# Kernel tuning notes

Hardware: AMD Instinct MI355X
Metric: run time of the kernel (lower is better)

Reference implementation:

```python
import jax, jax.numpy as jnp
import numpy as np

N_NODES = 100000
N_EDGES = 250000
EMB = 300
LAYERS = 5
BN_EPS = 1e-5


def setup_inputs() -> dict:
    key = jax.random.key(0)
    ks = jax.random.split(key, 16)
    inp = {
        "x": jax.random.randint(ks[0], (N_NODES, 2), 0, 3, dtype=jnp.int64) if jax.config.jax_enable_x64 else jax.random.randint(ks[0], (N_NODES, 2), 0, 3, dtype=jnp.int32),
        "edge_index": jax.random.randint(ks[1], (2, N_EDGES), 0, N_NODES, dtype=jnp.int32),
        "edge_attr": jax.random.randint(ks[2], (N_EDGES, 2), 0, 3, dtype=jnp.int32),
        "atom_emb1": jax.random.normal(ks[3], (120, EMB), jnp.float32) * 0.1,
        "atom_emb2": jax.random.normal(ks[4], (3, EMB), jnp.float32) * 0.1,
        "edge_emb1": jax.random.normal(ks[5], (LAYERS, 6, EMB), jnp.float32) * 0.1,
        "edge_emb2": jax.random.normal(ks[6], (LAYERS, 3, EMB), jnp.float32) * 0.1,
        "W1": jax.random.normal(ks[7], (LAYERS, EMB, 2 * EMB), jnp.float32) * (1.0 / np.sqrt(EMB)),
        "b1": jnp.zeros((LAYERS, 2 * EMB), jnp.float32),
        "W2": jax.random.normal(ks[8], (LAYERS, 2 * EMB, EMB), jnp.float32) * (1.0 / np.sqrt(2 * EMB)),
        "b2": jnp.zeros((LAYERS, EMB), jnp.float32),
        "gamma": jnp.ones((LAYERS, EMB), jnp.float32),
        "beta": jnp.zeros((LAYERS, EMB), jnp.float32),
    }
    return inp


def reference(x, edge_index, edge_attr, atom_emb1, atom_emb2, edge_emb1, edge_emb2,
              W1, b1, W2, b2, gamma, beta):
    N = x.shape[0]
    L = W1.shape[0]
    # AtomEncoder: sum of per-feature embeddings
    h = atom_emb1[x[:, 0]] + atom_emb2[x[:, 1]]  # [N, D]
    # add self loops (attr = (4, 0)); PyG: messages flow src=row0 -> dst=row1
    sl = jnp.arange(N, dtype=edge_index.dtype)
    src = jnp.concatenate([edge_index[0], sl])
    dst = jnp.concatenate([edge_index[1], sl])
    ea0 = jnp.concatenate([edge_attr[:, 0], jnp.full((N,), 4, edge_attr.dtype)])
    ea1 = jnp.concatenate([edge_attr[:, 1], jnp.zeros((N,), edge_attr.dtype)])
    for l in range(L):
        e = edge_emb1[l][ea0] + edge_emb2[l][ea1]           # [E+N, D]
        msg = h[src] + e                                     # gather + add
        agg = jax.ops.segment_sum(msg, dst, num_segments=N)  # scatter-add
        hmid = jax.nn.relu(agg @ W1[l] + b1[l])
        hout = hmid @ W2[l] + b2[l]
        mean = hout.mean(axis=0)
        var = hout.var(axis=0)
        hbn = (hout - mean) * jax.lax.rsqrt(var + BN_EPS) * gamma[l] + beta[l]
        h = hbn if l == L - 1 else jax.nn.relu(hbn)          # dropout ratio 0
    return h
```

## Files before the change

kernel.cpp:

```cpp
#include <hip/hip_runtime.h>
#include <hip/hip_bf16.h>

#define N_NODESC 100000
#define N_EDGESC 250000
#define EMB 300
#define LD 304
#define LD4 76
#define LAYERS 5
#define BN_EPS 1e-5f

#define K1 320
#define N1 640
#define K2 640
#define N2 384
#define HB 320

#define NB_SCAN 391

typedef __attribute__((ext_vector_type(8))) short short8;
typedef __attribute__((ext_vector_type(4))) float f32x4;

#define GLOAD16(g, l) __builtin_amdgcn_global_load_lds( \
    (const __attribute__((address_space(1))) void*)(g), \
    (__attribute__((address_space(3))) void*)(l), 16, 0, 0)

__device__ __forceinline__ float4 f4add(float4 a, float4 b){
    return make_float4(a.x+b.x, a.y+b.y, a.z+b.z, a.w+b.w);
}
__device__ __forceinline__ unsigned short f2bf(float f){
    __hip_bfloat16 h = __float2bfloat16(f);
    return *(unsigned short*)&h;
}
__device__ __forceinline__ float bf2f(unsigned short u){
    unsigned int x = ((unsigned int)u) << 16;
    union { unsigned int i; float f; } c; c.i = x; return c.f;
}

__global__ void k_zero_i(int* p, int n){
    int i = blockIdx.x*blockDim.x + threadIdx.x;
    if(i < n) p[i] = 0;
}
__global__ void k_zero_f(float* p, int n){
    int i = blockIdx.x*blockDim.x + threadIdx.x;
    if(i < n) p[i] = 0.f;
}

__global__ void k_atom(const int* __restrict__ x,
                       const float* __restrict__ e1,
                       const float* __restrict__ e2,
                       float* __restrict__ h){
    int idx = blockIdx.x*blockDim.x + threadIdx.x;
    if(idx >= N_NODESC*LD4) return;
    int i = idx / LD4, c = idx % LD4;
    float4 v = make_float4(0,0,0,0);
    if(c < 75){
        int i0 = x[2*i], i1 = x[2*i+1];
        const float4* r1 = (const float4*)(e1 + (size_t)i0*EMB);
        const float4* r2 = (const float4*)(e2 + (size_t)i1*EMB);
        v = f4add(r1[c], r2[c]);
    }
    ((float4*)h)[idx] = v;
}

__global__ void k_etab(const float* __restrict__ e1,
                       const float* __restrict__ e2,
                       float* __restrict__ etab){
    int idx = blockIdx.x*blockDim.x + threadIdx.x;
    if(idx >= LAYERS*18*LD4) return;
    int l = idx / (18*LD4);
    int r = idx % (18*LD4);
    int c = r / LD4, f = r % LD4;
    float4 v = make_float4(0,0,0,0);
    if(f < 75){
        const float4* r1 = (const float4*)(e1 + (size_t)(l*6 + c/3)*EMB);
        const float4* r2 = (const float4*)(e2 + (size_t)(l*3 + c%3)*EMB);
        v = f4add(r1[f], r2[f]);
    }
    ((float4*)etab)[idx] = v;
}

__global__ void k_prepw1(const float* __restrict__ W1, unsigned short* __restrict__ wb){
    int idx = blockIdx.x*blockDim.x + threadIdx.x;
    if(idx >= LAYERS*N1*K1) return;
    int l = idx / (N1*K1);
    int r = idx % (N1*K1);
    int n = r / K1, k = r % K1;
    float v = (n < 600 && k < EMB) ? W1[((size_t)l*EMB + k)*600 + n] : 0.f;
    wb[idx] = f2bf(v);
}
__global__ void k_prepw2(const float* __restrict__ W2, unsigned short* __restrict__ wb){
    int idx = blockIdx.x*blockDim.x + threadIdx.x;
    if(idx >= LAYERS*N2*K2) return;
    int l = idx / (N2*K2);
    int r = idx % (N2*K2);
    int n = r / K2, k = r % K2;
    float v = (n < EMB && k < 600) ? W2[((size_t)l*600 + k)*EMB + n] : 0.f;
    wb[idx] = f2bf(v);
}
__global__ void k_prepb1(const float* __restrict__ b1, float* __restrict__ bp){
    int idx = blockIdx.x*blockDim.x + threadIdx.x;
    if(idx >= LAYERS*N1) return;
    int l = idx / N1, n = idx % N1;
    bp[idx] = (n < 600) ? b1[(size_t)l*600 + n] : 0.f;
}

__global__ void k_deg(const int* __restrict__ ei, int* __restrict__ deg){
    int e = blockIdx.x*blockDim.x + threadIdx.x;
    if(e >= N_EDGESC) return;
    atomicAdd(&deg[ei[N_EDGESC + e]], 1);
}

__global__ void k_bsum(const int* __restrict__ deg, int* __restrict__ bsum){
    int g = blockIdx.x*256 + threadIdx.x;
    int v = (g < N_NODESC) ? deg[g] : 0;
    #pragma unroll
    for(int o=32;o>0;o>>=1) v += __shfl_down(v, o);
    __shared__ int sw[4];
    if((threadIdx.x & 63) == 0) sw[threadIdx.x>>6] = v;
    __syncthreads();
    if(threadIdx.x == 0) bsum[blockIdx.x] = sw[0]+sw[1]+sw[2]+sw[3];
}

__global__ void k_bscan(const int* __restrict__ bsum, int* __restrict__ bpre,
                        int* __restrict__ offs){
    __shared__ int sh[512];
    int t = threadIdx.x;
    int v = (t < NB_SCAN) ? bsum[t] : 0;
    sh[t] = v; __syncthreads();
    for(int o=1;o<512;o<<=1){
        int u = (t >= o) ? sh[t-o] : 0;
        __syncthreads();
        sh[t] += u;
        __syncthreads();
    }
    if(t < NB_SCAN) bpre[t] = sh[t] - v;
    if(t == NB_SCAN-1) offs[N_NODESC] = sh[t];
}

__global__ void k_offs(const int* __restrict__ deg, const int* __restrict__ bpre,
                       int* __restrict__ offs, int* __restrict__ cursor){
    __shared__ int sh[256];
    int t = threadIdx.x;
    int g = blockIdx.x*256 + t;
    int v = (g < N_NODESC) ? deg[g] : 0;
    sh[t] = v; __syncthreads();
    for(int o=1;o<256;o<<=1){
        int u = (t >= o) ? sh[t-o] : 0;
        __syncthreads();
        sh[t] += u;
        __syncthreads();
    }
    if(g < N_NODESC){
        int e = bpre[blockIdx.x] + sh[t] - v;
        offs[g] = e; cursor[g] = e;
    }
}

__global__ void k_fill(const int* __restrict__ ei, const int* __restrict__ ea,
                       int* __restrict__ cursor,
                       int* __restrict__ csr_src, int* __restrict__ csr_ea){
    int e = blockIdx.x*blockDim.x + threadIdx.x;
    if(e >= N_EDGESC) return;
    int d = ei[N_EDGESC + e];
    int p = atomicAdd(&cursor[d], 1);
    csr_src[p] = ei[e];
    csr_ea[p]  = ea[2*e]*3 + ea[2*e+1];
}

__global__ void k_agg0(const float* __restrict__ h, const float* __restrict__ etab_l,
                       const int* __restrict__ offs, const int* __restrict__ csr_src,
                       const int* __restrict__ csr_ea, unsigned short* __restrict__ agg){
    int idx = blockIdx.x*blockDim.x + threadIdx.x;
    if(idx >= N_NODESC*80) return;
    int i = idx / 80, c = idx % 80;
    ushort4 out;
    if(c < 75){
        const float4* h4 = (const float4*)h;
        const float4* et = (const float4*)etab_l;
        float4 acc = f4add(h4[(size_t)i*LD4 + c], et[12*LD4 + c]);
        int j0 = offs[i], j1 = offs[i+1];
        for(int j=j0; j<j1; j++){
            int s = csr_src[j];
            int t = csr_ea[j];
            acc = f4add(acc, f4add(h4[(size_t)s*LD4 + c], et[t*LD4 + c]));
        }
        out.x = f2bf(acc.x); out.y = f2bf(acc.y);
        out.z = f2bf(acc.z); out.w = f2bf(acc.w);
    } else {
        out.x = out.y = out.z = out.w = 0;
    }
    *(ushort4*)(agg + (size_t)i*K1 + c*4) = out;
}

__global__ void k_aggB(const unsigned short* __restrict__ src,
                       const float* __restrict__ etab_l,
                       const float* __restrict__ aff,
                       const int* __restrict__ offs, const int* __restrict__ csr_src,
                       const int* __restrict__ csr_ea, unsigned short* __restrict__ agg){
    int idx = blockIdx.x*blockDim.x + threadIdx.x;
    if(idx >= N_NODESC*80) return;
    int i = idx / 80, c = idx % 80;
    ushort4 out;
    if(c < 75){
        const float4* et = (const float4*)etab_l;
        float4 a4 = ((const float4*)aff)[c];
        float4 b4 = ((const float4*)aff)[75 + c];
        ushort4 sv = *(const ushort4*)(src + (size_t)i*HB + c*4);
        float4 e12 = et[12*LD4 + c];
        float4 acc;
        acc.x = fmaxf(fmaf(bf2f(sv.x), a4.x, b4.x), 0.f) + e12.x;
        acc.y = fmaxf(fmaf(bf2f(sv.y), a4.y, b4.y), 0.f) + e12.y;
        acc.z = fmaxf(fmaf(bf2f(sv.z), a4.z, b4.z), 0.f) + e12.z;
        acc.w = fmaxf(fmaf(bf2f(sv.w), a4.w, b4.w), 0.f) + e12.w;
        int j0 = offs[i], j1 = offs[i+1];
        for(int j=j0; j<j1; j++){
            int s = csr_src[j];
            int t = csr_ea[j];
            ushort4 nv = *(const ushort4*)(src + (size_t)s*HB + c*4);
            float4 ev = et[t*LD4 + c];
            acc.x += fmaxf(fmaf(bf2f(nv.x), a4.x, b4.x), 0.f) + ev.x;
            acc.y += fmaxf(fmaf(bf2f(nv.y), a4.y, b4.y), 0.f) + ev.y;
            acc.z += fmaxf(fmaf(bf2f(nv.z), a4.z, b4.z), 0.f) + ev.z;
            acc.w += fmaxf(fmaf(bf2f(nv.w), a4.w, b4.w), 0.f) + ev.w;
        }
        out.x = f2bf(acc.x); out.y = f2bf(acc.y);
        out.z = f2bf(acc.z); out.w = f2bf(acc.w);
    } else {
        out.x = out.y = out.z = out.w = 0;
    }
    *(ushort4*)(agg + (size_t)i*K1 + c*4) = out;
}

__global__ void k_bnaff(const float* __restrict__ stats, const float* __restrict__ g,
                        const float* __restrict__ bt, float* __restrict__ aff){
    int c = blockIdx.x*blockDim.x + threadIdx.x;
    if(c >= EMB) return;
    const float inv_n = 1.0f/(float)N_NODESC;
    float m = stats[c]*inv_n;
    float var = stats[EMB + c]*inv_n - m*m;
    float a = g[c]*rsqrtf(var + BN_EPS);
    aff[c] = a;
    aff[EMB + c] = bt[c] - m*a;
}

template<int EPI, int KS, int NX>
__global__ __launch_bounds__(512) void k_mgemm(
    const unsigned short* __restrict__ A,
    const unsigned short* __restrict__ Bt,
    const float* __restrict__ bias,
    void* __restrict__ Cptr, int M, int ldc,
    float* __restrict__ stats, int nwg)
{
    __shared__ char smem_c[3*16384 + 1024];
    unsigned short* smem_u = (unsigned short*)smem_c;

    int bid = blockIdx.x;
    int q = nwg >> 3, r = nwg & 7;
    int xcd = bid & 7, lo = bid >> 3;
    int wg = (xcd < r) ? (xcd*(q+1) + lo) : (r*(q+1) + (xcd - r)*q + lo);
    int bx = wg % NX, by = wg / NX;
    int m0 = by*128, n0 = bx*128;

    const int tid = threadIdx.x;
    const int wv = tid >> 6, ln = tid & 63;
    const int wvm = wv >> 2, wvn = wv & 3;
    const int lr = ln & 15, hi = ln >> 4;

    const int rS = tid >> 2, cS = tid & 3;
    int gA = m0 + rS; if(gA >= M) gA = M-1;
    const unsigned short* srcA = A  + (size_t)gA*(KS*32)        + ((cS ^ ((rS>>1)&3))<<3);
    const unsigned short* srcB = Bt + (size_t)(n0 + rS)*(KS*32) + ((cS ^ ((rS>>1)&3))<<3);

    f32x4 acc[4][2] = {};

    #define STAGE(t) { \
        char* db_ = smem_c + ((t)%3)*16384; \
        GLOAD16(srcA + (t)*32, db_ + tid*16); \
        GLOAD16(srcB + (t)*32, db_ + 8192 + tid*16); }

    STAGE(0)
    __builtin_amdgcn_sched_barrier(0);
    STAGE(1)
    __builtin_amdgcn_sched_barrier(0);

    int offA[4], offB[2];
    #pragma unroll
    for(int m=0;m<4;m++){
        int row = wvm*64 + m*16 + lr;
        offA[m] = row*32 + ((hi ^ ((row>>1)&3))<<3);
    }
    #pragma unroll
    for(int n=0;n<2;n++){
        int brow = wvn*32 + n*16 + lr;
        offB[n] = 4096 + brow*32 + ((hi ^ ((brow>>1)&3))<<3);
    }

    #pragma unroll
    for(int kc=0; kc<KS; kc++){
        if(kc == KS-1) asm volatile("s_waitcnt vmcnt(0) lgkmcnt(0)" ::: "memory");
        else           asm volatile("s_waitcnt vmcnt(2) lgkmcnt(0)" ::: "memory");
        __builtin_amdgcn_s_barrier();
        __builtin_amdgcn_sched_barrier(0);
        if(kc+2 < KS) STAGE(kc+2)
        const unsigned short* bufu = smem_u + (kc%3)*8192;
        short8 av[4], bv[2];
        #pragma unroll
        for(int m=0;m<4;m++) av[m] = *(const short8*)(bufu + offA[m]);
        #pragma unroll
        for(int n=0;n<2;n++) bv[n] = *(const short8*)(bufu + offB[n]);
        __builtin_amdgcn_s_setprio(1);
        #pragma unroll
        for(int m=0;m<4;m++)
            #pragma unroll
            for(int n=0;n<2;n++)
                acc[m][n] = __builtin_amdgcn_mfma_f32_16x16x32_bf16(
                                av[m], bv[n], acc[m][n], 0, 0, 0);
        __builtin_amdgcn_s_setprio(0);
    }
    #undef STAGE

    __syncthreads();

    if(EPI == 0){
        unsigned short* Cs = smem_u;
        unsigned short* Cb = (unsigned short*)Cptr;
        #pragma unroll
        for(int n=0;n<2;n++){
            int col = wvn*32 + n*16 + lr;
            float bsv = bias[n0 + col];
            #pragma unroll
            for(int m=0;m<4;m++){
                #pragma unroll
                for(int j=0;j<4;j++){
                    int row = wvm*64 + m*16 + hi*4 + j;
                    Cs[row*144 + col] = f2bf(fmaxf(acc[m][n][j] + bsv, 0.f));
                }
            }
        }
        __syncthreads();
        #pragma unroll
        for(int i=0;i<4;i++){
            int id = i*512 + tid;
            int rr = id >> 4, ch = id & 15;
            int gr = m0 + rr;
            if(gr < M)
                *(short8*)(Cb + (size_t)gr*ldc + n0 + ch*8) =
                    *(const short8*)(Cs + rr*144 + ch*8);
        }
    } else {
        float* red = (float*)(smem_c + 3*16384);
        #pragma unroll
        for(int n=0;n<2;n++){
            int col = n0 + wvn*32 + n*16 + lr;
            bool cok = (col < EMB);
            float bsv = cok ? bias[col] : 0.f;
            float sS = 0.f, sQ = 0.f;
            #pragma unroll
            for(int m=0;m<4;m++){
                #pragma unroll
                for(int j=0;j<4;j++){
                    int row = m0 + wvm*64 + m*16 + hi*4 + j;
                    if(cok && row < M){
                        float v = acc[m][n][j] + bsv;
                        sS += v; sQ += v*v;
                    }
                }
            }
            sS += __shfl_xor(sS, 16); sQ += __shfl_xor(sQ, 16);
            sS += __shfl_xor(sS, 32); sQ += __shfl_xor(sQ, 32);
            if(hi == 0){ red[(wv*16+lr)*2] = sS; red[(wv*16+lr)*2+1] = sQ; }
            __syncthreads();
            if(wv < 4 && ln < 16){
                float S = red[(wv*16+ln)*2]   + red[((wv+4)*16+ln)*2];
                float Q = red[(wv*16+ln)*2+1] + red[((wv+4)*16+ln)*2+1];
                int c2 = n0 + wv*32 + n*16 + ln;
                if(c2 < EMB){
                    atomicAdd(&stats[c2], S);
                    atomicAdd(&stats[EMB + c2], Q);
                }
            }
            __syncthreads();
        }
        if(EPI == 1){
            float* Cf = (float*)Cptr;
            float* Cs = (float*)smem_c;
            #pragma unroll
            for(int half=0; half<2; half++){
                if(wvm == half){
                    #pragma unroll
                    for(int n=0;n<2;n++){
                        int col = wvn*32 + n*16 + lr;
                        float bsv = (n0 + col < EMB) ? bias[n0 + col] : 0.f;
                        #pragma unroll
                        for(int m=0;m<4;m++){
                            #pragma unroll
                            for(int j=0;j<4;j++){
                                int rl = m*16 + hi*4 + j;
                                Cs[rl*132 + col] = acc[m][n][j] + bsv;
                            }
                        }
                    }
                }
                __syncthreads();
                #pragma unroll
                for(int i=0;i<4;i++){
                    int id = i*512 + tid;
                    int rr = id >> 5, c4 = id & 31;
                    int col = n0 + c4*4;
                    int gr = m0 + half*64 + rr;
                    if(col < EMB && gr < M)
                        *(float4*)(Cf + (size_t)gr*ldc + col) =
                            *(const float4*)(Cs + rr*132 + c4*4);
                }
                __syncthreads();
            }
        } else {
            unsigned short* Cs = smem_u;
            unsigned short* Cb = (unsigned short*)Cptr;
            #pragma unroll
            for(int n=0;n<2;n++){
                int col = wvn*32 + n*16 + lr;
                int gcol = n0 + col;
                bool cok = (gcol < EMB);
                float bsv = cok ? bias[gcol] : 0.f;
                #pragma unroll
                for(int m=0;m<4;m++){
                    #pragma unroll
                    for(int j=0;j<4;j++){
                        int row = wvm*64 + m*16 + hi*4 + j;
                        Cs[row*136 + col] =
                            cok ? f2bf(acc[m][n][j] + bsv) : (unsigned short)0;
                    }
                }
            }
            __syncthreads();
            #pragma unroll
            for(int i=0;i<4;i++){
                int id = i*512 + tid;
                int rr = id >> 4, ch = id & 15;
                int gr = m0 + rr;
                int gc = n0 + ch*8;
                if(gr < M && gc < HB)
                    *(short8*)(Cb + (size_t)gr*ldc + gc) =
                        *(const short8*)(Cs + rr*136 + ch*8);
            }
        }
    }
}

__global__ void k_bnapply(const float* __restrict__ X, const float* __restrict__ stats,
                          const float* __restrict__ g, const float* __restrict__ bt,
                          float* __restrict__ dout){
    int idx = blockIdx.x*blockDim.x + threadIdx.x;
    if(idx >= N_NODESC*75) return;
    int i = idx / 75, c = idx % 75;
    const float4* X4 = (const float4*)X;
    float4 v  = X4[(size_t)i*75 + c];
    float4 s  = ((const float4*)stats)[c];
    float4 q  = ((const float4*)stats)[75 + c];
    float4 gg = ((const float4*)g)[c];
    float4 bb = ((const float4*)bt)[c];
    const float inv_n = 1.0f/(float)N_NODESC;
    #define BN1(f) { float m = s.f*inv_n; float var = q.f*inv_n - m*m;          \
                     float r = rsqrtf(var + BN_EPS);                             \
                     v.f = (v.f - m)*r*gg.f + bb.f; }
    BN1(x) BN1(y) BN1(z) BN1(w)
    #undef BN1
    ((float4*)dout)[(size_t)i*75 + c] = v;
}

extern "C" void kernel_launch(void* const* d_in, const int* in_sizes, int n_in,
                              void* d_out, int out_size, void* d_ws, size_t ws_size,
                              hipStream_t stream) {
    const int*   x     = (const int*)d_in[0];
    const int*   ei    = (const int*)d_in[1];
    const int*   ea    = (const int*)d_in[2];
    const float* aemb1 = (const float*)d_in[3];
    const float* aemb2 = (const float*)d_in[4];
    const float* eemb1 = (const float*)d_in[5];
    const float* eemb2 = (const float*)d_in[6];
    const float* W1    = (const float*)d_in[7];
    const float* b1    = (const float*)d_in[8];
    const float* W2    = (const float*)d_in[9];
    const float* b2    = (const float*)d_in[10];
    const float* gamma = (const float*)d_in[11];
    const float* beta  = (const float*)d_in[12];
    float* dout = (float*)d_out;

    float* h      = (float*)d_ws;
    float* bias1p = h + (size_t)N_NODESC*LD;
    float* etab   = bias1p + LAYERS*N1;
    float* stats  = etab + LAYERS*18*LD;
    float* aff    = stats + 640;
    unsigned short* agg   = (unsigned short*)(aff + 640);
    unsigned short* hmid  = agg  + (size_t)N_NODESC*K1;
    unsigned short* houtb = hmid + (size_t)N_NODESC*N1;
    unsigned short* wb1t  = houtb + (size_t)N_NODESC*HB;
    unsigned short* wb2t  = wb1t + (size_t)LAYERS*N1*K1;
    int*   deg     = (int*)(wb2t + (size_t)LAYERS*N2*K2);
    int*   offs    = deg    + N_NODESC;
    int*   cursor  = offs   + N_NODESC + 1;
    int*   csr_src = cursor + N_NODESC + 1;
    int*   csr_ea  = csr_src + N_EDGESC;
    int*   bsum    = csr_ea + N_EDGESC;
    int*   bpre    = bsum + NB_SCAN;

    const int nb_nf4 = (N_NODESC*LD4 + 255)/256;

    k_atom<<<nb_nf4, 256, 0, stream>>>(x, aemb1, aemb2, h);
    k_etab<<<(LAYERS*18*LD4 + 255)/256, 256, 0, stream>>>(eemb1, eemb2, etab);
    k_prepw1<<<(LAYERS*N1*K1 + 255)/256, 256, 0, stream>>>(W1, wb1t);
    k_prepw2<<<(LAYERS*N2*K2 + 255)/256, 256, 0, stream>>>(W2, wb2t);
    k_prepb1<<<(LAYERS*N1 + 255)/256, 256, 0, stream>>>(b1, bias1p);
    k_zero_i<<<(N_NODESC + 255)/256, 256, 0, stream>>>(deg, N_NODESC);
    k_deg<<<(N_EDGESC + 255)/256, 256, 0, stream>>>(ei, deg);
    k_bsum<<<NB_SCAN, 256, 0, stream>>>(deg, bsum);
    k_bscan<<<1, 512, 0, stream>>>(bsum, bpre, offs);
    k_offs<<<NB_SCAN, 256, 0, stream>>>(deg, bpre, offs, cursor);
    k_fill<<<(N_EDGESC + 255)/256, 256, 0, stream>>>(ei, ea, cursor, csr_src, csr_ea);

    const int MT = (N_NODESC + 127)/128;
    const int nwg1 = 5*MT, nwg2 = 3*MT;
    const int nb_agg = (N_NODESC*80 + 255)/256;
    for(int l=0; l<LAYERS; l++){
        if(l == 0)
            k_agg0<<<nb_agg, 256, 0, stream>>>(
                h, etab, offs, csr_src, csr_ea, agg);
        else
            k_aggB<<<nb_agg, 256, 0, stream>>>(
                houtb, etab + (size_t)l*18*LD, aff, offs, csr_src, csr_ea, agg);
        k_zero_f<<<(2*EMB + 255)/256, 256, 0, stream>>>(stats, 2*EMB);
        k_mgemm<0, 10, 5><<<nwg1, 512, 0, stream>>>(
            agg, wb1t + (size_t)l*N1*K1, bias1p + (size_t)l*N1,
            hmid, N_NODESC, N1, nullptr, nwg1);
        if(l < LAYERS-1){
            k_mgemm<2, 20, 3><<<nwg2, 512, 0, stream>>>(
                hmid, wb2t + (size_t)l*N2*K2, b2 + (size_t)l*EMB,
                houtb, N_NODESC, HB, stats, nwg2);
            k_bnaff<<<2, 256, 0, stream>>>(stats, gamma + (size_t)l*EMB,
                                           beta + (size_t)l*EMB, aff);
        } else {
            k_mgemm<1, 20, 3><<<nwg2, 512, 0, stream>>>(
                hmid, wb2t + (size_t)l*N2*K2, b2 + (size_t)l*EMB,
                dout, N_NODESC, EMB, stats, nwg2);
            k_bnapply<<<(N_NODESC*75 + 255)/256, 256, 0, stream>>>(
                dout, stats, gamma + (size_t)l*EMB, beta + (size_t)l*EMB, dout);
        }
    }
}
```

Baseline: 1.165 ms.

## Use 4-wave GEMM blocks with 64x64 wave tiles and fold BN affine into aggregation

The MFMA GEMM drops from 8 waves (512 threads) to 4 waves (256 threads) per 128x128 tile. Each wave now computes a 64x64 subtile with 4x4 accumulators and issues twice as many async global-to-LDS loads per stage. The batch-norm statistic reduction is restructured so all column groups sync once instead of once per group. The separate k_bnaff launch is removed: each aggregation thread recomputes the BN scale and shift from the raw stats, gamma and beta. This trades a kernel launch for redundant per-thread rsqrt work, and the GEMM change raises register pressure in exchange for more operand reuse per wave.

Result: no change. 1.172 ms (+0.6%).

```diff
diff --git a/kernel.cpp b/kernel.cpp
--- a/kernel.cpp
+++ b/kernel.cpp
@@ -194,7 +194,9 @@
 
 __global__ void k_aggB(const unsigned short* __restrict__ src,
                        const float* __restrict__ etab_l,
-                       const float* __restrict__ aff,
+                       const float* __restrict__ stats,
+                       const float* __restrict__ gam,
+                       const float* __restrict__ bet,
                        const int* __restrict__ offs, const int* __restrict__ csr_src,
                        const int* __restrict__ csr_ea, unsigned short* __restrict__ agg){
     int idx = blockIdx.x*blockDim.x + threadIdx.x;
@@ -203,8 +205,18 @@
     ushort4 out;
     if(c < 75){
         const float4* et = (const float4*)etab_l;
-        float4 a4 = ((const float4*)aff)[c];
-        float4 b4 = ((const float4*)aff)[75 + c];
+        const float inv_n = 1.0f/(float)N_NODESC;
+        float4 s4 = ((const float4*)stats)[c];
+        float4 q4 = ((const float4*)stats)[75 + c];
+        float4 g4 = ((const float4*)gam)[c];
+        float4 t4 = ((const float4*)bet)[c];
+        float4 a4, b4;
+        #define MKAFF(f) { float m_ = s4.f*inv_n;                                 \
+                           float var_ = q4.f*inv_n - m_*m_;                       \
+                           a4.f = g4.f*rsqrtf(var_ + BN_EPS);                     \
+                           b4.f = t4.f - m_*a4.f; }
+        MKAFF(x) MKAFF(y) MKAFF(z) MKAFF(w)
+        #undef MKAFF
         ushort4 sv = *(const ushort4*)(src + (size_t)i*HB + c*4);
         float4 e12 = et[12*LD4 + c];
         float4 acc;
@@ -231,27 +243,15 @@
     *(ushort4*)(agg + (size_t)i*K1 + c*4) = out;
 }
 
-__global__ void k_bnaff(const float* __restrict__ stats, const float* __restrict__ g,
-                        const float* __restrict__ bt, float* __restrict__ aff){
-    int c = blockIdx.x*blockDim.x + threadIdx.x;
-    if(c >= EMB) return;
-    const float inv_n = 1.0f/(float)N_NODESC;
-    float m = stats[c]*inv_n;
-    float var = stats[EMB + c]*inv_n - m*m;
-    float a = g[c]*rsqrtf(var + BN_EPS);
-    aff[c] = a;
-    aff[EMB + c] = bt[c] - m*a;
-}
-
 template<int EPI, int KS, int NX>
-__global__ __launch_bounds__(512) void k_mgemm(
+__global__ __launch_bounds__(256, 3) void k_mgemm(
     const unsigned short* __restrict__ A,
     const unsigned short* __restrict__ Bt,
     const float* __restrict__ bias,
     void* __restrict__ Cptr, int M, int ldc,
     float* __restrict__ stats, int nwg)
 {
-    __shared__ char smem_c[3*16384 + 1024];
+    __shared__ char smem_c[3*16384 + 2048];
     unsigned short* smem_u = (unsigned short*)smem_c;
 
     int bid = blockIdx.x;
@@ -263,56 +263,63 @@
 
     const int tid = threadIdx.x;
     const int wv = tid >> 6, ln = tid & 63;
-    const int wvm = wv >> 2, wvn = wv & 3;
+    const int wvm = wv >> 1, wvn = wv & 1;
     const int lr = ln & 15, hi = ln >> 4;
 
-    const int rS = tid >> 2, cS = tid & 3;
-    int gA = m0 + rS; if(gA >= M) gA = M-1;
-    const unsigned short* srcA = A  + (size_t)gA*(KS*32)        + ((cS ^ ((rS>>1)&3))<<3);
-    const unsigned short* srcB = Bt + (size_t)(n0 + rS)*(KS*32) + ((cS ^ ((rS>>1)&3))<<3);
-
-    f32x4 acc[4][2] = {};
+    const int id0 = tid, id1 = tid + 256;
+    const int rA0 = id0 >> 2, rA1 = id1 >> 2;
+    const int c0 = id0 & 3,  c1 = id1 & 3;
+    int g0 = m0 + rA0; if(g0 >= M) g0 = M-1;
+    int g1 = m0 + rA1; if(g1 >= M) g1 = M-1;
+    const unsigned short* srcA0 = A  + (size_t)g0*(KS*32) + ((c0 ^ ((rA0>>1)&3))<<3);
+    const unsigned short* srcA1 = A  + (size_t)g1*(KS*32) + ((c1 ^ ((rA1>>1)&3))<<3);
+    const unsigned short* srcB0 = Bt + (size_t)(n0 + rA0)*(KS*32) + ((c0 ^ ((rA0>>1)&3))<<3);
+    const unsigned short* srcB1 = Bt + (size_t)(n0 + rA1)*(KS*32) + ((c1 ^ ((rA1>>1)&3))<<3);
+
+    f32x4 acc[4][4] = {};
 
     #define STAGE(t) { \
         char* db_ = smem_c + ((t)%3)*16384; \
-        GLOAD16(srcA + (t)*32, db_ + tid*16); \
-        GLOAD16(srcB + (t)*32, db_ + 8192 + tid*16); }
+        GLOAD16(srcA0 + (t)*32, db_ + id0*16); \
+        GLOAD16(srcA1 + (t)*32, db_ + id1*16); \
+        GLOAD16(srcB0 + (t)*32, db_ + 8192 + id0*16); \
+        GLOAD16(srcB1 + (t)*32, db_ + 8192 + id1*16); }
 
     STAGE(0)
     __builtin_amdgcn_sched_barrier(0);
     STAGE(1)
     __builtin_amdgcn_sched_barrier(0);
 
-    int offA[4], offB[2];
+    int offA[4], offB[4];
     #pragma unroll
     for(int m=0;m<4;m++){
         int row = wvm*64 + m*16 + lr;
         offA[m] = row*32 + ((hi ^ ((row>>1)&3))<<3);
     }
     #pragma unroll
-    for(int n=0;n<2;n++){
-        int brow = wvn*32 + n*16 + lr;
+    for(int n=0;n<4;n++){
+        int brow = wvn*64 + n*16 + lr;
         offB[n] = 4096 + brow*32 + ((hi ^ ((brow>>1)&3))<<3);
     }
 
     #pragma unroll
     for(int kc=0; kc<KS; kc++){
         if(kc == KS-1) asm volatile("s_waitcnt vmcnt(0) lgkmcnt(0)" ::: "memory");
-        else           asm volatile("s_waitcnt vmcnt(2) lgkmcnt(0)" ::: "memory");
+        else           asm volatile("s_waitcnt vmcnt(4) lgkmcnt(0)" ::: "memory");
         __builtin_amdgcn_s_barrier();
         __builtin_amdgcn_sched_barrier(0);
         if(kc+2 < KS) STAGE(kc+2)
         const unsigned short* bufu = smem_u + (kc%3)*8192;
-        short8 av[4], bv[2];
+        short8 av[4], bv[4];
         #pragma unroll
         for(int m=0;m<4;m++) av[m] = *(const short8*)(bufu + offA[m]);
         #pragma unroll
-        for(int n=0;n<2;n++) bv[n] = *(const short8*)(bufu + offB[n]);
+        for(int n=0;n<4;n++) bv[n] = *(const short8*)(bufu + offB[n]);
         __builtin_amdgcn_s_setprio(1);
         #pragma unroll
         for(int m=0;m<4;m++)
             #pragma unroll
-            for(int n=0;n<2;n++)
+            for(int n=0;n<4;n++)
                 acc[m][n] = __builtin_amdgcn_mfma_f32_16x16x32_bf16(
                                 av[m], bv[n], acc[m][n], 0, 0, 0);
         __builtin_amdgcn_s_setprio(0);
@@ -325,8 +332,8 @@
         unsigned short* Cs = smem_u;
         unsigned short* Cb = (unsigned short*)Cptr;
         #pragma unroll
-        for(int n=0;n<2;n++){
-            int col = wvn*32 + n*16 + lr;
+        for(int n=0;n<4;n++){
+            int col = wvn*64 + n*16 + lr;
             float bsv = bias[n0 + col];
             #pragma unroll
             for(int m=0;m<4;m++){
@@ -339,8 +346,8 @@
         }
         __syncthreads();
         #pragma unroll
-        for(int i=0;i<4;i++){
-            int id = i*512 + tid;
+        for(int i=0;i<8;i++){
+            int id = i*256 + tid;
             int rr = id >> 4, ch = id & 15;
             int gr = m0 + rr;
             if(gr < M)
@@ -350,8 +357,8 @@
     } else {
         float* red = (float*)(smem_c + 3*16384);
         #pragma unroll
-        for(int n=0;n<2;n++){
-            int col = n0 + wvn*32 + n*16 + lr;
+        for(int n=0;n<4;n++){
+            int col = n0 + wvn*64 + n*16 + lr;
             bool cok = (col < EMB);
             float bsv = cok ? bias[col] : 0.f;
             float sS = 0.f, sQ = 0.f;
@@ -368,19 +375,24 @@
             }
             sS += __shfl_xor(sS, 16); sQ += __shfl_xor(sQ, 16);
             sS += __shfl_xor(sS, 32); sQ += __shfl_xor(sQ, 32);
-            if(hi == 0){ red[(wv*16+lr)*2] = sS; red[(wv*16+lr)*2+1] = sQ; }
-            __syncthreads();
-            if(wv < 4 && ln < 16){
-                float S = red[(wv*16+ln)*2]   + red[((wv+4)*16+ln)*2];
-                float Q = red[(wv*16+ln)*2+1] + red[((wv+4)*16+ln)*2+1];
-                int c2 = n0 + wv*32 + n*16 + ln;
-                if(c2 < EMB){
-                    atomicAdd(&stats[c2], S);
-                    atomicAdd(&stats[EMB + c2], Q);
-                }
-            }
-            __syncthreads();
-        }
+            if(hi == 0){
+                red[(wv*4+n)*16 + lr]       = sS;
+                red[256 + (wv*4+n)*16 + lr] = sQ;
+            }
+        }
+        __syncthreads();
+        if(tid < 128){
+            int twvn = tid >> 6, tn = (tid >> 4) & 3, tlr = tid & 15;
+            float S = red[(twvn*4+tn)*16 + tlr] + red[((2+twvn)*4+tn)*16 + tlr];
+            float Q = red[256 + (twvn*4+tn)*16 + tlr]
+                    + red[256 + ((2+twvn)*4+tn)*16 + tlr];
+            int c2 = n0 + twvn*64 + tn*16 + tlr;
+            if(c2 < EMB){
+                atomicAdd(&stats[c2], S);
+                atomicAdd(&stats[EMB + c2], Q);
+            }
+        }
+        __syncthreads();
         if(EPI == 1){
             float* Cf = (float*)Cptr;
             float* Cs = (float*)smem_c;
@@ -388,8 +400,8 @@
             for(int half=0; half<2; half++){
                 if(wvm == half){
                     #pragma unroll
-                    for(int n=0;n<2;n++){
-                        int col = wvn*32 + n*16 + lr;
+                    for(int n=0;n<4;n++){
+                        int col = wvn*64 + n*16 + lr;
                         float bsv = (n0 + col < EMB) ? bias[n0 + col] : 0.f;
                         #pragma unroll
                         for(int m=0;m<4;m++){
@@ -403,8 +415,8 @@
                 }
                 __syncthreads();
                 #pragma unroll
-                for(int i=0;i<4;i++){
-                    int id = i*512 + tid;
+                for(int i=0;i<8;i++){
+                    int id = i*256 + tid;
                     int rr = id >> 5, c4 = id & 31;
                     int col = n0 + c4*4;
                     int gr = m0 + half*64 + rr;
@@ -418,8 +430,8 @@
             unsigned short* Cs = smem_u;
             unsigned short* Cb = (unsigned short*)Cptr;
             #pragma unroll
-            for(int n=0;n<2;n++){
-                int col = wvn*32 + n*16 + lr;
+            for(int n=0;n<4;n++){
+                int col = wvn*64 + n*16 + lr;
                 int gcol = n0 + col;
                 bool cok = (gcol < EMB);
                 float bsv = cok ? bias[gcol] : 0.f;
@@ -435,8 +447,8 @@
             }
             __syncthreads();
             #pragma unroll
-            for(int i=0;i<4;i++){
-                int id = i*512 + tid;
+            for(int i=0;i<8;i++){
+                int id = i*256 + tid;
                 int rr = id >> 4, ch = id & 15;
                 int gr = m0 + rr;
                 int gc = n0 + ch*8;
@@ -528,19 +540,19 @@
                 h, etab, offs, csr_src, csr_ea, agg);
         else
             k_aggB<<<nb_agg, 256, 0, stream>>>(
-                houtb, etab + (size_t)l*18*LD, aff, offs, csr_src, csr_ea, agg);
+                houtb, etab + (size_t)l*18*LD, stats,
+                gamma + (size_t)(l-1)*EMB, beta + (size_t)(l-1)*EMB,
+                offs, csr_src, csr_ea, agg);
         k_zero_f<<<(2*EMB + 255)/256, 256, 0, stream>>>(stats, 2*EMB);
-        k_mgemm<0, 10, 5><<<nwg1, 512, 0, stream>>>(
+        k_mgemm<0, 10, 5><<<nwg1, 256, 0, stream>>>(
             agg, wb1t + (size_t)l*N1*K1, bias1p + (size_t)l*N1,
             hmid, N_NODESC, N1, nullptr, nwg1);
         if(l < LAYERS-1){
-            k_mgemm<2, 20, 3><<<nwg2, 512, 0, stream>>>(
+            k_mgemm<2, 20, 3><<<nwg2, 256, 0, stream>>>(
                 hmid, wb2t + (size_t)l*N2*K2, b2 + (size_t)l*EMB,
                 houtb, N_NODESC, HB, stats, nwg2);
-            k_bnaff<<<2, 256, 0, stream>>>(stats, gamma + (size_t)l*EMB,
-                                           beta + (size_t)l*EMB, aff);
         } else {
-            k_mgemm<1, 20, 3><<<nwg2, 512, 0, stream>>>(
+            k_mgemm<1, 20, 3><<<nwg2, 256, 0, stream>>>(
                 hmid, wb2t + (size_t)l*N2*K2, b2 + (size_t)l*EMB,
                 dout, N_NODESC, EMB, stats, nwg2);
             k_bnapply<<<(N_NODESC*75 + 255)/256, 256, 0, stream>>>(
```

## Widen GEMM K-tile to 64 with double buffering and fold BN affine into aggregation

Applied to the files above, without the earlier changes.

The MFMA GEMM now stages 64-wide K tiles in two 32 KB LDS buffers, using an 8-way XOR swizzle, instead of 32-wide tiles in three buffers. This halves the number of barrier and wait iterations per tile. In exchange, each iteration waits for all outstanding loads, so only one stage is prefetched ahead. Separately, the per-layer BN affine kernel is removed: each aggregation thread recomputes scale and shift from the raw stats, gamma and beta, which saves one small launch per layer.

New measurement: 1.196 ms. 1.03x slower.

```diff
diff --git a/kernel.cpp b/kernel.cpp
--- a/kernel.cpp
+++ b/kernel.cpp
@@ -194,7 +194,9 @@
 
 __global__ void k_aggB(const unsigned short* __restrict__ src,
                        const float* __restrict__ etab_l,
-                       const float* __restrict__ aff,
+                       const float* __restrict__ stats,
+                       const float* __restrict__ gam,
+                       const float* __restrict__ bet,
                        const int* __restrict__ offs, const int* __restrict__ csr_src,
                        const int* __restrict__ csr_ea, unsigned short* __restrict__ agg){
     int idx = blockIdx.x*blockDim.x + threadIdx.x;
@@ -203,8 +205,18 @@
     ushort4 out;
     if(c < 75){
         const float4* et = (const float4*)etab_l;
-        float4 a4 = ((const float4*)aff)[c];
-        float4 b4 = ((const float4*)aff)[75 + c];
+        const float inv_n = 1.0f/(float)N_NODESC;
+        float4 s4 = ((const float4*)stats)[c];
+        float4 q4 = ((const float4*)stats)[75 + c];
+        float4 g4 = ((const float4*)gam)[c];
+        float4 t4 = ((const float4*)bet)[c];
+        float4 a4, b4;
+        #define MKAFF(f) { float m_ = s4.f*inv_n;                                 \
+                           float var_ = q4.f*inv_n - m_*m_;                       \
+                           a4.f = g4.f*rsqrtf(var_ + BN_EPS);                     \
+                           b4.f = t4.f - m_*a4.f; }
+        MKAFF(x) MKAFF(y) MKAFF(z) MKAFF(w)
+        #undef MKAFF
         ushort4 sv = *(const ushort4*)(src + (size_t)i*HB + c*4);
         float4 e12 = et[12*LD4 + c];
         float4 acc;
@@ -231,18 +243,6 @@
     *(ushort4*)(agg + (size_t)i*K1 + c*4) = out;
 }
 
-__global__ void k_bnaff(const float* __restrict__ stats, const float* __restrict__ g,
-                        const float* __restrict__ bt, float* __restrict__ aff){
-    int c = blockIdx.x*blockDim.x + threadIdx.x;
-    if(c >= EMB) return;
-    const float inv_n = 1.0f/(float)N_NODESC;
-    float m = stats[c]*inv_n;
-    float var = stats[EMB + c]*inv_n - m*m;
-    float a = g[c]*rsqrtf(var + BN_EPS);
-    aff[c] = a;
-    aff[EMB + c] = bt[c] - m*a;
-}
-
 template<int EPI, int KS, int NX>
 __global__ __launch_bounds__(512) void k_mgemm(
     const unsigned short* __restrict__ A,
@@ -251,8 +251,9 @@
     void* __restrict__ Cptr, int M, int ldc,
     float* __restrict__ stats, int nwg)
 {
-    __shared__ char smem_c[3*16384 + 1024];
+    __shared__ char smem_c[65536];
     unsigned short* smem_u = (unsigned short*)smem_c;
+    constexpr int KDIM = KS*64;
 
     int bid = blockIdx.x;
     int q = nwg >> 3, r = nwg & 7;
@@ -266,56 +267,66 @@
     const int wvm = wv >> 2, wvn = wv & 3;
     const int lr = ln & 15, hi = ln >> 4;
 
-    const int rS = tid >> 2, cS = tid & 3;
-    int gA = m0 + rS; if(gA >= M) gA = M-1;
-    const unsigned short* srcA = A  + (size_t)gA*(KS*32)        + ((cS ^ ((rS>>1)&3))<<3);
-    const unsigned short* srcB = Bt + (size_t)(n0 + rS)*(KS*32) + ((cS ^ ((rS>>1)&3))<<3);
+    const int id0 = tid, id1 = tid + 512;
+    const int rA0 = id0 >> 3, rA1 = id1 >> 3;
+    const int c80 = id0 & 7,  c81 = id1 & 7;
+    int g0 = m0 + rA0; if(g0 >= M) g0 = M-1;
+    int g1 = m0 + rA1; if(g1 >= M) g1 = M-1;
+    const unsigned short* srcA0 = A  + (size_t)g0*KDIM + ((c80 ^ (rA0&7))<<3);
+    const unsigned short* srcA1 = A  + (size_t)g1*KDIM + ((c81 ^ (rA1&7))<<3);
+    const unsigned short* srcB0 = Bt + (size_t)(n0 + rA0)*KDIM + ((c80 ^ (rA0&7))<<3);
+    const unsigned short* srcB1 = Bt + (size_t)(n0 + rA1)*KDIM + ((c81 ^ (rA1&7))<<3);
 
     f32x4 acc[4][2] = {};
 
     #define STAGE(t) { \
-        char* db_ = smem_c + ((t)%3)*16384; \
-        GLOAD16(srcA + (t)*32, db_ + tid*16); \
-        GLOAD16(srcB + (t)*32, db_ + 8192 + tid*16); }
+        char* db_ = smem_c + ((t)&1)*32768; \
+        GLOAD16(srcA0 + (t)*64, db_ + id0*16); \
+        GLOAD16(srcA1 + (t)*64, db_ + id1*16); \
+        GLOAD16(srcB0 + (t)*64, db_ + 16384 + id0*16); \
+        GLOAD16(srcB1 + (t)*64, db_ + 16384 + id1*16); }
 
     STAGE(0)
     __builtin_amdgcn_sched_barrier(0);
-    STAGE(1)
-    __builtin_amdgcn_sched_barrier(0);
-
-    int offA[4], offB[2];
+
+    int offA[2][4], offB[2][2];
     #pragma unroll
-    for(int m=0;m<4;m++){
-        int row = wvm*64 + m*16 + lr;
-        offA[m] = row*32 + ((hi ^ ((row>>1)&3))<<3);
-    }
-    #pragma unroll
-    for(int n=0;n<2;n++){
-        int brow = wvn*32 + n*16 + lr;
-        offB[n] = 4096 + brow*32 + ((hi ^ ((brow>>1)&3))<<3);
+    for(int kh=0;kh<2;kh++){
+        #pragma unroll
+        for(int m=0;m<4;m++){
+            int row = wvm*64 + m*16 + lr;
+            offA[kh][m] = row*64 + (((kh*4 + hi) ^ (row&7))<<3);
+        }
+        #pragma unroll
+        for(int n=0;n<2;n++){
+            int brow = wvn*32 + n*16 + lr;
+            offB[kh][n] = 8192 + brow*64 + (((kh*4 + hi) ^ (brow&7))<<3);
+        }
     }
 
     #pragma unroll
     for(int kc=0; kc<KS; kc++){
-        if(kc == KS-1) asm volatile("s_waitcnt vmcnt(0) lgkmcnt(0)" ::: "memory");
-        else           asm volatile("s_waitcnt vmcnt(2) lgkmcnt(0)" ::: "memory");
+        asm volatile("s_waitcnt vmcnt(0) lgkmcnt(0)" ::: "memory");
         __builtin_amdgcn_s_barrier();
         __builtin_amdgcn_sched_barrier(0);
-        if(kc+2 < KS) STAGE(kc+2)
-        const unsigned short* bufu = smem_u + (kc%3)*8192;
-        short8 av[4], bv[2];
+        if(kc+1 < KS) STAGE(kc+1)
+        const unsigned short* bufu = smem_u + (kc&1)*16384;
         #pragma unroll
-        for(int m=0;m<4;m++) av[m] = *(const short8*)(bufu + offA[m]);
-        #pragma unroll
-        for(int n=0;n<2;n++) bv[n] = *(const short8*)(bufu + offB[n]);
-        __builtin_amdgcn_s_setprio(1);
-        #pragma unroll
-        for(int m=0;m<4;m++)
-            #pragma unroll
-            for(int n=0;n<2;n++)
-                acc[m][n] = __builtin_amdgcn_mfma_f32_16x16x32_bf16(
-                                av[m], bv[n], acc[m][n], 0, 0, 0);
-        __builtin_amdgcn_s_setprio(0);
+        for(int kh=0;kh<2;kh++){
+            short8 av[4], bv[2];
+            #pragma unroll
+            for(int m=0;m<4;m++) av[m] = *(const short8*)(bufu + offA[kh][m]);
+            #pragma unroll
+            for(int n=0;n<2;n++) bv[n] = *(const short8*)(bufu + offB[kh][n]);
+            __builtin_amdgcn_s_setprio(1);
+            #pragma unroll
+            for(int m=0;m<4;m++)
+                #pragma unroll
+                for(int n=0;n<2;n++)
+                    acc[m][n] = __builtin_amdgcn_mfma_f32_16x16x32_bf16(
+                                    av[m], bv[n], acc[m][n], 0, 0, 0);
+            __builtin_amdgcn_s_setprio(0);
+        }
     }
     #undef STAGE
 
@@ -348,7 +359,7 @@
                     *(const short8*)(Cs + rr*144 + ch*8);
         }
     } else {
-        float* red = (float*)(smem_c + 3*16384);
+        float* red = (float*)(smem_c + 40960);
         #pragma unroll
         for(int n=0;n<2;n++){
             int col = n0 + wvn*32 + n*16 + lr;
@@ -528,19 +539,19 @@
                 h, etab, offs, csr_src, csr_ea, agg);
         else
             k_aggB<<<nb_agg, 256, 0, stream>>>(
-                houtb, etab + (size_t)l*18*LD, aff, offs, csr_src, csr_ea, agg);
+                houtb, etab + (size_t)l*18*LD, stats,
+                gamma + (size_t)(l-1)*EMB, beta + (size_t)(l-1)*EMB,
+                offs, csr_src, csr_ea, agg);
         k_zero_f<<<(2*EMB + 255)/256, 256, 0, stream>>>(stats, 2*EMB);
-        k_mgemm<0, 10, 5><<<nwg1, 512, 0, stream>>>(
+        k_mgemm<0, 5, 5><<<nwg1, 512, 0, stream>>>(
             agg, wb1t + (size_t)l*N1*K1, bias1p + (size_t)l*N1,
             hmid, N_NODESC, N1, nullptr, nwg1);
         if(l < LAYERS-1){
-            k_mgemm<2, 20, 3><<<nwg2, 512, 0, stream>>>(
+            k_mgemm<2, 10, 3><<<nwg2, 512, 0, stream>>>(
                 hmid, wb2t + (size_t)l*N2*K2, b2 + (size_t)l*EMB,
                 houtb, N_NODESC, HB, stats, nwg2);
-            k_bnaff<<<2, 256, 0, stream>>>(stats, gamma + (size_t)l*EMB,
-                                           beta + (size_t)l*EMB, aff);
         } else {
-            k_mgemm<1, 20, 3><<<nwg2, 512, 0, stream>>>(
+            k_mgemm<1, 10, 3><<<nwg2, 512, 0, stream>>>(
                 hmid, wb2t + (size_t)l*N2*K2, b2 + (size_t)l*EMB,
                 dout, N_NODESC, EMB, stats, nwg2);
             k_bnapply<<<(N_NODESC*75 + 255)/256, 256, 0, stream>>>(
```
